# Performance work log

Measured on AMD Instinct MI355X. Metric: run time of the kernel, lower is better.

Reference implementation:

```python
import jax, jax.numpy as jnp
import numpy as np

IN_DIMS = 512
TOKEN_DIM = 512
NUM_HEADS = 1
D = TOKEN_DIM * NUM_HEADS
SCALE = TOKEN_DIM ** (-0.5)
EPS = 1e-12  # torch F.normalize default


def _l2norm(v, axis):
    n = jnp.sqrt(jnp.sum(v * v, axis=axis, keepdims=True))
    return v / jnp.maximum(n, EPS)


def setup_inputs() -> dict:
    key = jax.random.key(0)
    ks = jax.random.split(key, 10)
    B, C, H, W = 64, IN_DIMS, 28, 28
    s_in = IN_DIMS ** -0.5
    s_d = D ** -0.5
    return {
        "x": jax.random.normal(ks[0], (B, C, H, W), jnp.float32),
        "Wq": jax.random.normal(ks[1], (IN_DIMS, D), jnp.float32) * s_in,
        "bq": jax.random.normal(ks[2], (D,), jnp.float32) * 0.01,
        "Wk": jax.random.normal(ks[3], (IN_DIMS, D), jnp.float32) * s_in,
        "bk": jax.random.normal(ks[4], (D,), jnp.float32) * 0.01,
        "w_g": jax.random.normal(ks[5], (D, 1), jnp.float32),
        "Wp": jax.random.normal(ks[6], (D, D), jnp.float32) * s_d,
        "bp": jax.random.normal(ks[7], (D,), jnp.float32) * 0.01,
        "Wf": jax.random.normal(ks[8], (D, TOKEN_DIM), jnp.float32) * s_d,
        "bf": jax.random.normal(ks[9], (TOKEN_DIM,), jnp.float32) * 0.01,
    }


def reference(x, Wq, bq, Wk, bk, w_g, Wp, bp, Wf, bf):
    B, C, H, W = x.shape
    t = x.reshape(B, C, H * W).transpose(0, 2, 1)          # [B, N, C]
    query = _l2norm(t @ Wq + bq, axis=-1)                  # [B, N, D]
    k = _l2norm(t @ Wk + bk, axis=-1)                      # [B, N, D]
    attn = _l2norm((query @ w_g) * SCALE, axis=1)          # [B, N, 1], normalized over tokens
    ctx = jnp.sum(attn * query, axis=1, keepdims=True)     # [B, 1, D] global context
    out = (ctx * k) @ Wp + bp + query                      # [B, N, D]
    out = out @ Wf + bf                                    # [B, N, TOKEN_DIM]
    return out.transpose(0, 2, 1).reshape(B, -1, H, W)
```

## Files before the change

kernel.cpp:

```cpp
#include <hip/hip_runtime.h>

#define EPSN 1e-12f
#define SCALE_F 0.044194173824159216f
#define MTOT 50176

typedef __bf16 bf16x8 __attribute__((ext_vector_type(8)));
typedef __bf16 bf16x4 __attribute__((ext_vector_type(4)));
typedef float  f32x4  __attribute__((ext_vector_type(4)));

__device__ __forceinline__ void gld16(const void* src, void* dst) {
  __builtin_amdgcn_global_load_lds(
      (const __attribute__((address_space(1))) unsigned int*)src,
      (__attribute__((address_space(3))) unsigned int*)dst, 16, 0, 0);
}

__global__ __launch_bounds__(256) void k_prep_t(const float* __restrict__ Wq,
                                                const float* __restrict__ Wk,
                                                __bf16* __restrict__ WqT,
                                                __bf16* __restrict__ WkT) {
  __shared__ float Tq[32][33], Tk[32][33];
  const int c0 = blockIdx.x * 32, d0 = blockIdx.y * 32;
  const int dx = threadIdx.x, cy = threadIdx.y;
  #pragma unroll
  for (int p = 0; p < 4; ++p) {
    int c = cy + p * 8;
    Tq[c][dx] = Wq[(size_t)(c0 + c) * 512 + d0 + dx];
    Tk[c][dx] = Wk[(size_t)(c0 + c) * 512 + d0 + dx];
  }
  __syncthreads();
  #pragma unroll
  for (int p = 0; p < 4; ++p) {
    int d = cy + p * 8;
    WqT[(size_t)(d0 + d) * 512 + c0 + dx] = (__bf16)Tq[dx][d];
    WkT[(size_t)(d0 + d) * 512 + c0 + dx] = (__bf16)Tk[dx][d];
  }
}

__global__ __launch_bounds__(512) void k_prep_w(const float* __restrict__ Wp,
                                                const float* __restrict__ Wf,
                                                const float* __restrict__ bp,
                                                const float* __restrict__ bfv,
                                                __bf16* __restrict__ WcT,
                                                float* __restrict__ bpf) {
  const int kk0 = blockIdx.x * 8;
  const int d = threadIdx.x;
  float acc[8] = {};
  float bacc = 0.f;
  const bool dobp = (blockIdx.x == 0);
  for (int c = 0; c < 512; ++c) {
    float wf = Wf[(size_t)c * 512 + d];
    #pragma unroll
    for (int i = 0; i < 8; ++i) acc[i] = fmaf(Wp[(size_t)(kk0 + i) * 512 + c], wf, acc[i]);
    if (dobp) bacc = fmaf(bp[c], wf, bacc);
  }
  #pragma unroll
  for (int i = 0; i < 8; ++i) {
    WcT[(size_t)d * 1024 + kk0 + i]       = (__bf16)acc[i];
    WcT[(size_t)d * 1024 + 512 + kk0 + i] = (__bf16)Wf[(size_t)(kk0 + i) * 512 + d];
  }
  if (dobp) bpf[d] = bacc + bfv[d];
}

__global__ __launch_bounds__(256, 3) void k_gemm(const float* __restrict__ x,
                                                 const __bf16* __restrict__ WqT,
                                                 const __bf16* __restrict__ WkT,
                                                 const float* __restrict__ bq,
                                                 const float* __restrict__ bk,
                                                 const float* __restrict__ wg,
                                                 __bf16* __restrict__ qraw,
                                                 __bf16* __restrict__ kraw,
                                                 float* __restrict__ psqQ,
                                                 float* __restrict__ psqK,
                                                 float* __restrict__ gdo) {
  __shared__ __align__(1024) unsigned char As[8192], Bs[8192];
  const int t = threadIdx.x, l = t & 63, w = t >> 6;
  const int li = l & 15, lq = l >> 4;
  const int p = blockIdx.x;
  const int xq = p & 7, q2 = p >> 3;
  const int m8 = q2 & 7;
  const int g = (q2 >> 3) * 8 + xq;
  const int b = g / 7, mt = g % 7;
  const int qk = m8 >> 2, nt = m8 & 3;
  const int m0 = mt * 128;
  const __bf16* Wt = qk ? WkT : WqT;

  const int r0 = 2 * w, r1 = r0 + 1;
  int row0 = m0 + r0 * 16 + li; if (row0 > 783) row0 = 783;
  int row1 = m0 + r1 * 16 + li; if (row1 > 783) row1 = 783;
  const float* xp0 = x + ((size_t)b * 512 + lq * 8) * 784 + row0;
  const float* xp1 = x + ((size_t)b * 512 + lq * 8) * 784 + row1;
  const __bf16* wp0 = Wt + (size_t)(nt * 128 + r0 * 16 + li) * 512 + lq * 8;
  const __bf16* wp1 = Wt + (size_t)(nt * 128 + r1 * 16 + li) * 512 + lq * 8;

  f32x4 acc[4][4] = {};

  for (int ks = 0; ks < 16; ++ks) {
    const int k0 = ks * 32;
    gld16(wp0 + k0, Bs + r0 * 1024);
    gld16(wp1 + k0, Bs + r1 * 1024);
    {
      float v0[8], v1[8];
      #pragma unroll
      for (int j = 0; j < 8; ++j) v0[j] = xp0[(size_t)(k0 + j) * 784];
      #pragma unroll
      for (int j = 0; j < 8; ++j) v1[j] = xp1[(size_t)(k0 + j) * 784];
      bf16x8 a0, a1;
      #pragma unroll
      for (int j = 0; j < 8; ++j) { a0[j] = (__bf16)v0[j]; a1[j] = (__bf16)v1[j]; }
      *(bf16x8*)(As + r0 * 1024 + l * 16) = a0;
      *(bf16x8*)(As + r1 * 1024 + l * 16) = a1;
    }
    __syncthreads();
    bf16x8 af[4];
    #pragma unroll
    for (int rb = 0; rb < 4; ++rb)
      af[rb] = *(const bf16x8*)(As + ((w & 1) * 4 + rb) * 1024 + l * 16);
    #pragma unroll
    for (int cb = 0; cb < 4; ++cb) {
      bf16x8 bf = *(const bf16x8*)(Bs + ((w >> 1) * 4 + cb) * 1024 + l * 16);
      #pragma unroll
      for (int rb = 0; rb < 4; ++rb)
        acc[rb][cb] = __builtin_amdgcn_mfma_f32_16x16x32_bf16(af[rb], bf, acc[rb][cb], 0, 0, 0);
    }
    __syncthreads();
  }

  const float* bias = qk ? bk : bq;
  __bf16* dst = qk ? kraw : qraw;
  float* psq = qk ? psqK : psqQ;
  const int colb = nt * 128 + (w >> 1) * 64;
  const int cg = nt * 2 + (w >> 1);
  float bv[4], wv[4];
  #pragma unroll
  for (int cb = 0; cb < 4; ++cb) {
    int col = colb + cb * 16 + li;
    bv[cb] = bias[col];
    wv[cb] = qk ? 0.f : wg[col];
  }
  #pragma unroll
  for (int rb = 0; rb < 4; ++rb)
    #pragma unroll
    for (int j = 0; j < 4; ++j) {
      int rowg = m0 + (w & 1) * 64 + rb * 16 + lq * 4 + j;
      bool ok = rowg < 784;
      size_t token = (size_t)b * 784 + rowg;
      float ss = 0.f, sg = 0.f;
      #pragma unroll
      for (int cb = 0; cb < 4; ++cb) {
        float v = acc[rb][cb][j] + bv[cb];
        ss = fmaf(v, v, ss);
        sg = fmaf(v, wv[cb], sg);
        if (ok) dst[token * 512 + colb + cb * 16 + li] = (__bf16)v;
      }
      ss += __shfl_xor(ss, 1); ss += __shfl_xor(ss, 2); ss += __shfl_xor(ss, 4); ss += __shfl_xor(ss, 8);
      sg += __shfl_xor(sg, 1); sg += __shfl_xor(sg, 2); sg += __shfl_xor(sg, 4); sg += __shfl_xor(sg, 8);
      if (ok && li == 0) {
        psq[(size_t)cg * MTOT + token] = ss;
        if (!qk) gdo[(size_t)cg * MTOT + token] = sg;
      }
    }
}

__global__ __launch_bounds__(256) void k_normc(const float* __restrict__ psqQ,
                                               const float* __restrict__ psqK,
                                               const float* __restrict__ gdo,
                                               float* __restrict__ invqA,
                                               float* __restrict__ invkA,
                                               float* __restrict__ coefA,
                                               float* __restrict__ gA) {
  const int tkn = blockIdx.x * 256 + threadIdx.x;
  if (tkn >= MTOT) return;
  float sq = 0.f, sk = 0.f, gd = 0.f;
  #pragma unroll
  for (int cg = 0; cg < 8; ++cg) {
    sq += psqQ[(size_t)cg * MTOT + tkn];
    sk += psqK[(size_t)cg * MTOT + tkn];
    gd += gdo[(size_t)cg * MTOT + tkn];
  }
  float invq = 1.f / fmaxf(sqrtf(sq), EPSN);
  float invk = 1.f / fmaxf(sqrtf(sk), EPSN);
  float gv = gd * invq;
  invqA[tkn] = invq;
  invkA[tkn] = invk;
  coefA[tkn] = gv * invq;
  gA[tkn]    = gv;
}

__global__ __launch_bounds__(512) void k_pctx(const __bf16* __restrict__ qraw,
                                              const float* __restrict__ coefA,
                                              const float* __restrict__ gA,
                                              float* __restrict__ ctx) {
  __shared__ float wred[8];
  const int b = blockIdx.x, t = threadIdx.x;
  const size_t base = (size_t)b * 784;
  float gsq = 0.f;
  { float gv = gA[base + t]; gsq = gv * gv; }
  if (t + 512 < 784) { float gv = gA[base + t + 512]; gsq = fmaf(gv, gv, gsq); }
  gsq += __shfl_xor(gsq, 1);  gsq += __shfl_xor(gsq, 2);  gsq += __shfl_xor(gsq, 4);
  gsq += __shfl_xor(gsq, 8);  gsq += __shfl_xor(gsq, 16); gsq += __shfl_xor(gsq, 32);
  if ((t & 63) == 0) wred[t >> 6] = gsq;
  __syncthreads();
  float tot = 0.f;
  #pragma unroll
  for (int i = 0; i < 8; ++i) tot += wred[i];
  const float alpha = SCALE_F / fmaxf(sqrtf(tot) * SCALE_F, EPSN);
  float a0 = 0.f, a1 = 0.f, a2 = 0.f, a3 = 0.f;
  for (int n = 0; n < 784; n += 4) {
    a0 = fmaf(coefA[base + n],     (float)qraw[(base + n) * 512 + t],     a0);
    a1 = fmaf(coefA[base + n + 1], (float)qraw[(base + n + 1) * 512 + t], a1);
    a2 = fmaf(coefA[base + n + 2], (float)qraw[(base + n + 2) * 512 + t], a2);
    a3 = fmaf(coefA[base + n + 3], (float)qraw[(base + n + 3) * 512 + t], a3);
  }
  ctx[(size_t)b * 512 + t] = alpha * ((a0 + a1) + (a2 + a3));
}

__global__ __launch_bounds__(256, 3) void k_out(const __bf16* __restrict__ qraw,
                                                const __bf16* __restrict__ kraw,
                                                const float* __restrict__ invqA,
                                                const float* __restrict__ invkA,
                                                const float* __restrict__ ctx,
                                                const __bf16* __restrict__ WcT,
                                                const float* __restrict__ bpf,
                                                float* __restrict__ out) {
  __shared__ __align__(1024) unsigned char As[8192], Bs[8192];
  __shared__ float ctx_l[512];
  const int t = threadIdx.x, l = t & 63, w = t >> 6;
  const int li = l & 15, lq = l >> 4;
  const int p = blockIdx.x;
  const int xq = p & 7, q2 = p >> 3;
  const int nt = q2 & 3;
  const int g = (q2 >> 2) * 8 + xq;
  const int b = g / 7, mt = g % 7;
  const int m0 = mt * 128;

  ctx_l[t]       = ctx[(size_t)b * 512 + t];
  ctx_l[t + 256] = ctx[(size_t)b * 512 + t + 256];

  const int rA0 = w, rA1 = w + 4;
  int row0 = m0 + rA0 * 16 + li; if (row0 > 783) row0 = 783;
  int row1 = m0 + rA1 * 16 + li; if (row1 > 783) row1 = 783;
  const size_t tk0 = (size_t)b * 784 + row0, tk1 = (size_t)b * 784 + row1;
  const float iq0 = invqA[tk0], ik0 = invkA[tk0];
  const float iq1 = invqA[tk1], ik1 = invkA[tk1];
  const __bf16* wpB0 = WcT + (size_t)(nt * 128 + (2 * w) * 16 + li) * 1024 + lq * 8;
  const __bf16* wpB1 = WcT + (size_t)(nt * 128 + (2 * w + 1) * 16 + li) * 1024 + lq * 8;

  f32x4 acc[4][4] = {};
  __syncthreads();

  for (int ks = 0; ks < 32; ++ks) {
    const int k0 = ks * 32;
    gld16(wpB0 + k0, Bs + (2 * w) * 1024);
    gld16(wpB1 + k0, Bs + (2 * w + 1) * 1024);
    {
      const bool dk = ks < 16;
      const __bf16* ap = dk ? kraw : qraw;
      const int kk = (k0 & 511) + lq * 8;
      bf16x8 v0 = *(const bf16x8*)(ap + tk0 * 512 + kk);
      bf16x8 v1 = *(const bf16x8*)(ap + tk1 * 512 + kk);
      const float s0 = dk ? ik0 : iq0, s1 = dk ? ik1 : iq1;
      bf16x8 o0, o1;
      if (dk) {
        f32x4 c0 = *(const f32x4*)&ctx_l[kk];
        f32x4 c1 = *(const f32x4*)&ctx_l[kk + 4];
        #pragma unroll
        for (int j = 0; j < 4; ++j) {
          o0[j]     = (__bf16)((float)v0[j]     * s0 * c0[j]);
          o0[4 + j] = (__bf16)((float)v0[4 + j] * s0 * c1[j]);
          o1[j]     = (__bf16)((float)v1[j]     * s1 * c0[j]);
          o1[4 + j] = (__bf16)((float)v1[4 + j] * s1 * c1[j]);
        }
      } else {
        #pragma unroll
        for (int j = 0; j < 8; ++j) {
          o0[j] = (__bf16)((float)v0[j] * s0);
          o1[j] = (__bf16)((float)v1[j] * s1);
        }
      }
      *(bf16x8*)(As + rA0 * 1024 + l * 16) = o0;
      *(bf16x8*)(As + rA1 * 1024 + l * 16) = o1;
    }
    __syncthreads();
    bf16x8 af[4];
    #pragma unroll
    for (int rb = 0; rb < 4; ++rb)
      af[rb] = *(const bf16x8*)(As + ((w & 1) * 4 + rb) * 1024 + l * 16);
    #pragma unroll
    for (int cb = 0; cb < 4; ++cb) {
      bf16x8 bf = *(const bf16x8*)(Bs + ((w >> 1) * 4 + cb) * 1024 + l * 16);
      #pragma unroll
      for (int rb = 0; rb < 4; ++rb)
        acc[rb][cb] = __builtin_amdgcn_mfma_f32_16x16x32_bf16(af[rb], bf, acc[rb][cb], 0, 0, 0);
    }
    __syncthreads();
  }

  const int colb = nt * 128 + (w >> 1) * 64;
  float bv[4];
  #pragma unroll
  for (int cb = 0; cb < 4; ++cb) bv[cb] = bpf[colb + cb * 16 + li];
  #pragma unroll
  for (int rb = 0; rb < 4; ++rb) {
    int nrow = m0 + (w & 1) * 64 + rb * 16 + lq * 4;
    if (nrow < 784) {
      #pragma unroll
      for (int cb = 0; cb < 4; ++cb) {
        f32x4 v;
        #pragma unroll
        for (int j = 0; j < 4; ++j) v[j] = acc[rb][cb][j] + bv[cb];
        *(f32x4*)&out[((size_t)b * 512 + colb + cb * 16 + li) * 784 + nrow] = v;
      }
    }
  }
}

extern "C" void kernel_launch(void* const* d_in, const int* in_sizes, int n_in,
                              void* d_out, int out_size, void* d_ws, size_t ws_size,
                              hipStream_t stream) {
  const float* x   = (const float*)d_in[0];
  const float* Wq  = (const float*)d_in[1];
  const float* bq  = (const float*)d_in[2];
  const float* Wk  = (const float*)d_in[3];
  const float* bk  = (const float*)d_in[4];
  const float* wg  = (const float*)d_in[5];
  const float* Wp  = (const float*)d_in[6];
  const float* bp  = (const float*)d_in[7];
  const float* Wf  = (const float*)d_in[8];
  const float* bfv = (const float*)d_in[9];
  float* out = (float*)d_out;
  char* ws = (char*)d_ws;

  const size_t SZRAW = (size_t)MTOT * 512 * 2;
  size_t off = 0;
  __bf16* qraw = (__bf16*)(ws + off); off += SZRAW;
  __bf16* kraw = (__bf16*)(ws + off); off += SZRAW;
  __bf16* WqT  = (__bf16*)(ws + off); off += 524288;
  __bf16* WkT  = (__bf16*)(ws + off); off += 524288;
  __bf16* WcT  = (__bf16*)(ws + off); off += 1048576;
  float*  bpf  = (float*) (ws + off); off += 2048;
  float*  psqQ = (float*) (ws + off); off += (size_t)8 * MTOT * 4;
  float*  psqK = (float*) (ws + off); off += (size_t)8 * MTOT * 4;
  float*  gdo  = (float*) (ws + off); off += (size_t)8 * MTOT * 4;
  float*  invqA = (float*)(ws + off); off += (size_t)MTOT * 4;
  float*  invkA = (float*)(ws + off); off += (size_t)MTOT * 4;
  float*  coefA = (float*)(ws + off); off += (size_t)MTOT * 4;
  float*  gA    = (float*)(ws + off); off += (size_t)MTOT * 4;
  float*  ctx   = (float*)(ws + off); off += 131072;

  k_prep_t<<<dim3(16, 16), dim3(32, 8), 0, stream>>>(Wq, Wk, WqT, WkT);
  k_prep_w<<<dim3(64),     dim3(512),   0, stream>>>(Wp, Wf, bp, bfv, WcT, bpf);
  k_gemm  <<<dim3(3584),   dim3(256),   0, stream>>>(x, WqT, WkT, bq, bk, wg,
                                                     qraw, kraw, psqQ, psqK, gdo);
  k_normc <<<dim3(196),    dim3(256),   0, stream>>>(psqQ, psqK, gdo, invqA, invkA, coefA, gA);
  k_pctx  <<<dim3(64),     dim3(512),   0, stream>>>(qraw, coefA, gA, ctx);
  k_out   <<<dim3(1792),   dim3(256),   0, stream>>>(qraw, kraw, invqA, invkA, ctx, WcT, bpf, out);
}
```

Baseline: 411.3 us.

## Pre-transpose x to bf16, fuse Q/K GEMMs, and split ctx reduction

Adds a transpose kernel that writes x as token-major bf16 in two half-batch chunks. The GEMM then loads A tiles with direct global-to-LDS loads instead of strided fp32 loads plus conversion. The GEMM now computes Q and K together from one shared A tile, halving the number of x reads at the cost of doubled accumulators, higher register pressure and occupancy lowered to 2. The context kernel is split across 4 channel chunks and 4 token slices per batch to expose more parallelism. The risk is the extra round trip through the transpose buffer.

```diff
diff --git a/kernel.cpp b/kernel.cpp
--- a/kernel.cpp
+++ b/kernel.cpp
@@ -5,13 +5,33 @@
 #define MTOT 50176
 
 typedef __bf16 bf16x8 __attribute__((ext_vector_type(8)));
-typedef __bf16 bf16x4 __attribute__((ext_vector_type(4)));
 typedef float  f32x4  __attribute__((ext_vector_type(4)));
 
 __device__ __forceinline__ void gld16(const void* src, void* dst) {
   __builtin_amdgcn_global_load_lds(
       (const __attribute__((address_space(1))) unsigned int*)src,
       (__attribute__((address_space(3))) unsigned int*)dst, 16, 0, 0);
+}
+
+__global__ __launch_bounds__(256) void k_xt(const float* __restrict__ x,
+                                            __bf16* __restrict__ xT, int b0) {
+  __shared__ float T[32][33];
+  const int n0 = blockIdx.x * 32, c0 = blockIdx.y * 32;
+  const int bl = blockIdx.z, b = b0 + bl;
+  const int dx = threadIdx.x, ty = threadIdx.y;
+  #pragma unroll
+  for (int pp = 0; pp < 4; ++pp) {
+    int c = ty + pp * 8;
+    int n = n0 + dx;
+    T[c][dx] = (n < 784) ? x[((size_t)b * 512 + c0 + c) * 784 + n] : 0.f;
+  }
+  __syncthreads();
+  #pragma unroll
+  for (int pp = 0; pp < 4; ++pp) {
+    int n = ty + pp * 8;
+    if (n0 + n < 784)
+      xT[((size_t)bl * 784 + n0 + n) * 512 + c0 + dx] = (__bf16)T[dx][n];
+  }
 }
 
 __global__ __launch_bounds__(256) void k_prep_t(const float* __restrict__ Wq,
@@ -61,55 +81,49 @@
   if (dobp) bpf[d] = bacc + bfv[d];
 }
 
-__global__ __launch_bounds__(256, 3) void k_gemm(const float* __restrict__ x,
+__global__ __launch_bounds__(256, 2) void k_gemm(const __bf16* __restrict__ xT,
                                                  const __bf16* __restrict__ WqT,
                                                  const __bf16* __restrict__ WkT,
                                                  const float* __restrict__ bq,
                                                  const float* __restrict__ bk,
                                                  const float* __restrict__ wg,
+                                                 const int b0,
                                                  __bf16* __restrict__ qraw,
                                                  __bf16* __restrict__ kraw,
                                                  float* __restrict__ psqQ,
                                                  float* __restrict__ psqK,
                                                  float* __restrict__ gdo) {
-  __shared__ __align__(1024) unsigned char As[8192], Bs[8192];
+  __shared__ __align__(1024) unsigned char As[8192], BQs[8192], BKs[8192];
   const int t = threadIdx.x, l = t & 63, w = t >> 6;
   const int li = l & 15, lq = l >> 4;
   const int p = blockIdx.x;
   const int xq = p & 7, q2 = p >> 3;
-  const int m8 = q2 & 7;
-  const int g = (q2 >> 3) * 8 + xq;
-  const int b = g / 7, mt = g % 7;
-  const int qk = m8 >> 2, nt = m8 & 3;
+  const int nt = q2 & 3;
+  const int g = (q2 >> 2) * 8 + xq;
+  const int bl = g / 7, mt = g % 7;
+  const int b = b0 + bl;
   const int m0 = mt * 128;
-  const __bf16* Wt = qk ? WkT : WqT;
 
   const int r0 = 2 * w, r1 = r0 + 1;
   int row0 = m0 + r0 * 16 + li; if (row0 > 783) row0 = 783;
   int row1 = m0 + r1 * 16 + li; if (row1 > 783) row1 = 783;
-  const float* xp0 = x + ((size_t)b * 512 + lq * 8) * 784 + row0;
-  const float* xp1 = x + ((size_t)b * 512 + lq * 8) * 784 + row1;
-  const __bf16* wp0 = Wt + (size_t)(nt * 128 + r0 * 16 + li) * 512 + lq * 8;
-  const __bf16* wp1 = Wt + (size_t)(nt * 128 + r1 * 16 + li) * 512 + lq * 8;
-
-  f32x4 acc[4][4] = {};
+  const __bf16* a0s = xT + ((size_t)bl * 784 + row0) * 512 + lq * 8;
+  const __bf16* a1s = xT + ((size_t)bl * 784 + row1) * 512 + lq * 8;
+  const __bf16* q0s = WqT + (size_t)(nt * 128 + r0 * 16 + li) * 512 + lq * 8;
+  const __bf16* q1s = WqT + (size_t)(nt * 128 + r1 * 16 + li) * 512 + lq * 8;
+  const __bf16* k0s = WkT + (size_t)(nt * 128 + r0 * 16 + li) * 512 + lq * 8;
+  const __bf16* k1s = WkT + (size_t)(nt * 128 + r1 * 16 + li) * 512 + lq * 8;
+
+  f32x4 accQ[4][4] = {}, accK[4][4] = {};
 
   for (int ks = 0; ks < 16; ++ks) {
     const int k0 = ks * 32;
-    gld16(wp0 + k0, Bs + r0 * 1024);
-    gld16(wp1 + k0, Bs + r1 * 1024);
-    {
-      float v0[8], v1[8];
-      #pragma unroll
-      for (int j = 0; j < 8; ++j) v0[j] = xp0[(size_t)(k0 + j) * 784];
-      #pragma unroll
-      for (int j = 0; j < 8; ++j) v1[j] = xp1[(size_t)(k0 + j) * 784];
-      bf16x8 a0, a1;
-      #pragma unroll
-      for (int j = 0; j < 8; ++j) { a0[j] = (__bf16)v0[j]; a1[j] = (__bf16)v1[j]; }
-      *(bf16x8*)(As + r0 * 1024 + l * 16) = a0;
-      *(bf16x8*)(As + r1 * 1024 + l * 16) = a1;
-    }
+    gld16(a0s + k0, As + r0 * 1024);
+    gld16(a1s + k0, As + r1 * 1024);
+    gld16(q0s + k0, BQs + r0 * 1024);
+    gld16(q1s + k0, BQs + r1 * 1024);
+    gld16(k0s + k0, BKs + r0 * 1024);
+    gld16(k1s + k0, BKs + r1 * 1024);
     __syncthreads();
     bf16x8 af[4];
     #pragma unroll
@@ -117,25 +131,25 @@
       af[rb] = *(const bf16x8*)(As + ((w & 1) * 4 + rb) * 1024 + l * 16);
     #pragma unroll
     for (int cb = 0; cb < 4; ++cb) {
-      bf16x8 bf = *(const bf16x8*)(Bs + ((w >> 1) * 4 + cb) * 1024 + l * 16);
+      bf16x8 bq8 = *(const bf16x8*)(BQs + ((w >> 1) * 4 + cb) * 1024 + l * 16);
       #pragma unroll
       for (int rb = 0; rb < 4; ++rb)
-        acc[rb][cb] = __builtin_amdgcn_mfma_f32_16x16x32_bf16(af[rb], bf, acc[rb][cb], 0, 0, 0);
+        accQ[rb][cb] = __builtin_amdgcn_mfma_f32_16x16x32_bf16(af[rb], bq8, accQ[rb][cb], 0, 0, 0);
+      bf16x8 bk8 = *(const bf16x8*)(BKs + ((w >> 1) * 4 + cb) * 1024 + l * 16);
+      #pragma unroll
+      for (int rb = 0; rb < 4; ++rb)
+        accK[rb][cb] = __builtin_amdgcn_mfma_f32_16x16x32_bf16(af[rb], bk8, accK[rb][cb], 0, 0, 0);
     }
     __syncthreads();
   }
 
-  const float* bias = qk ? bk : bq;
-  __bf16* dst = qk ? kraw : qraw;
-  float* psq = qk ? psqK : psqQ;
   const int colb = nt * 128 + (w >> 1) * 64;
   const int cg = nt * 2 + (w >> 1);
-  float bv[4], wv[4];
+  float bqv[4], bkv[4], wv[4];
   #pragma unroll
   for (int cb = 0; cb < 4; ++cb) {
     int col = colb + cb * 16 + li;
-    bv[cb] = bias[col];
-    wv[cb] = qk ? 0.f : wg[col];
+    bqv[cb] = bq[col]; bkv[cb] = bk[col]; wv[cb] = wg[col];
   }
   #pragma unroll
   for (int rb = 0; rb < 4; ++rb)
@@ -144,19 +158,26 @@
       int rowg = m0 + (w & 1) * 64 + rb * 16 + lq * 4 + j;
       bool ok = rowg < 784;
       size_t token = (size_t)b * 784 + rowg;
-      float ss = 0.f, sg = 0.f;
+      float ssq = 0.f, ssk = 0.f, sg = 0.f;
       #pragma unroll
       for (int cb = 0; cb < 4; ++cb) {
-        float v = acc[rb][cb][j] + bv[cb];
-        ss = fmaf(v, v, ss);
-        sg = fmaf(v, wv[cb], sg);
-        if (ok) dst[token * 512 + colb + cb * 16 + li] = (__bf16)v;
+        float vq = accQ[rb][cb][j] + bqv[cb];
+        float vk = accK[rb][cb][j] + bkv[cb];
+        ssq = fmaf(vq, vq, ssq);
+        ssk = fmaf(vk, vk, ssk);
+        sg  = fmaf(vq, wv[cb], sg);
+        if (ok) {
+          qraw[token * 512 + colb + cb * 16 + li] = (__bf16)vq;
+          kraw[token * 512 + colb + cb * 16 + li] = (__bf16)vk;
+        }
       }
-      ss += __shfl_xor(ss, 1); ss += __shfl_xor(ss, 2); ss += __shfl_xor(ss, 4); ss += __shfl_xor(ss, 8);
-      sg += __shfl_xor(sg, 1); sg += __shfl_xor(sg, 2); sg += __shfl_xor(sg, 4); sg += __shfl_xor(sg, 8);
+      ssq += __shfl_xor(ssq, 1); ssq += __shfl_xor(ssq, 2); ssq += __shfl_xor(ssq, 4); ssq += __shfl_xor(ssq, 8);
+      ssk += __shfl_xor(ssk, 1); ssk += __shfl_xor(ssk, 2); ssk += __shfl_xor(ssk, 4); ssk += __shfl_xor(ssk, 8);
+      sg  += __shfl_xor(sg, 1);  sg  += __shfl_xor(sg, 2);  sg  += __shfl_xor(sg, 4);  sg  += __shfl_xor(sg, 8);
       if (ok && li == 0) {
-        psq[(size_t)cg * MTOT + token] = ss;
-        if (!qk) gdo[(size_t)cg * MTOT + token] = sg;
+        psqQ[(size_t)cg * MTOT + token] = ssq;
+        psqK[(size_t)cg * MTOT + token] = ssk;
+        gdo [(size_t)cg * MTOT + token] = sg;
       }
     }
 }
@@ -191,9 +212,10 @@
                                               const float* __restrict__ gA,
                                               float* __restrict__ ctx) {
   __shared__ float wred[8];
-  const int b = blockIdx.x, t = threadIdx.x;
+  __shared__ float part[4][128];
+  const int ch = blockIdx.x, b = blockIdx.y, t = threadIdx.x;
   const size_t base = (size_t)b * 784;
-  float gsq = 0.f;
+  float gsq;
   { float gv = gA[base + t]; gsq = gv * gv; }
   if (t + 512 < 784) { float gv = gA[base + t + 512]; gsq = fmaf(gv, gv, gsq); }
   gsq += __shfl_xor(gsq, 1);  gsq += __shfl_xor(gsq, 2);  gsq += __shfl_xor(gsq, 4);
@@ -204,14 +226,23 @@
   #pragma unroll
   for (int i = 0; i < 8; ++i) tot += wred[i];
   const float alpha = SCALE_F / fmaxf(sqrtf(tot) * SCALE_F, EPSN);
+  const int dof = t & 127, s = t >> 7;
+  const int nb = s * 196;
+  const __bf16* qb = qraw + (base + nb) * 512 + ch * 128 + dof;
+  const float* cf = coefA + base + nb;
   float a0 = 0.f, a1 = 0.f, a2 = 0.f, a3 = 0.f;
-  for (int n = 0; n < 784; n += 4) {
-    a0 = fmaf(coefA[base + n],     (float)qraw[(base + n) * 512 + t],     a0);
-    a1 = fmaf(coefA[base + n + 1], (float)qraw[(base + n + 1) * 512 + t], a1);
-    a2 = fmaf(coefA[base + n + 2], (float)qraw[(base + n + 2) * 512 + t], a2);
-    a3 = fmaf(coefA[base + n + 3], (float)qraw[(base + n + 3) * 512 + t], a3);
-  }
-  ctx[(size_t)b * 512 + t] = alpha * ((a0 + a1) + (a2 + a3));
+  for (int n = 0; n < 196; n += 4) {
+    a0 = fmaf(cf[n],     (float)qb[(size_t)n * 512],       a0);
+    a1 = fmaf(cf[n + 1], (float)qb[(size_t)(n + 1) * 512], a1);
+    a2 = fmaf(cf[n + 2], (float)qb[(size_t)(n + 2) * 512], a2);
+    a3 = fmaf(cf[n + 3], (float)qb[(size_t)(n + 3) * 512], a3);
+  }
+  part[s][dof] = (a0 + a1) + (a2 + a3);
+  __syncthreads();
+  if (t < 128) {
+    float sum = part[0][t] + part[1][t] + part[2][t] + part[3][t];
+    ctx[(size_t)b * 512 + ch * 128 + t] = alpha * sum;
+  }
 }
 
 __global__ __launch_bounds__(256, 3) void k_out(const __bf16* __restrict__ qraw,
@@ -331,9 +362,11 @@
   char* ws = (char*)d_ws;
 
   const size_t SZRAW = (size_t)MTOT * 512 * 2;
+  const size_t SZXT  = (size_t)32 * 784 * 512 * 2;
   size_t off = 0;
   __bf16* qraw = (__bf16*)(ws + off); off += SZRAW;
   __bf16* kraw = (__bf16*)(ws + off); off += SZRAW;
+  __bf16* xT   = (__bf16*)(ws + off); off += SZXT;
   __bf16* WqT  = (__bf16*)(ws + off); off += 524288;
   __bf16* WkT  = (__bf16*)(ws + off); off += 524288;
   __bf16* WcT  = (__bf16*)(ws + off); off += 1048576;
@@ -349,9 +382,12 @@
 
   k_prep_t<<<dim3(16, 16), dim3(32, 8), 0, stream>>>(Wq, Wk, WqT, WkT);
   k_prep_w<<<dim3(64),     dim3(512),   0, stream>>>(Wp, Wf, bp, bfv, WcT, bpf);
-  k_gemm  <<<dim3(3584),   dim3(256),   0, stream>>>(x, WqT, WkT, bq, bk, wg,
-                                                     qraw, kraw, psqQ, psqK, gdo);
-  k_normc <<<dim3(196),    dim3(256),   0, stream>>>(psqQ, psqK, gdo, invqA, invkA, coefA, gA);
-  k_pctx  <<<dim3(64),     dim3(512),   0, stream>>>(qraw, coefA, gA, ctx);
-  k_out   <<<dim3(1792),   dim3(256),   0, stream>>>(qraw, kraw, invqA, invkA, ctx, WcT, bpf, out);
-}
+  for (int s = 0; s < 2; ++s) {
+    k_xt  <<<dim3(25, 16, 32), dim3(32, 8), 0, stream>>>(x, xT, s * 32);
+    k_gemm<<<dim3(896),        dim3(256),   0, stream>>>(xT, WqT, WkT, bq, bk, wg, s * 32,
+                                                         qraw, kraw, psqQ, psqK, gdo);
+  }
+  k_normc<<<dim3(196),   dim3(256), 0, stream>>>(psqQ, psqK, gdo, invqA, invkA, coefA, gA);
+  k_pctx <<<dim3(4, 64), dim3(512), 0, stream>>>(qraw, coefA, gA, ctx);
+  k_out  <<<dim3(1792),  dim3(256), 0, stream>>>(qraw, kraw, invqA, invkA, ctx, WcT, bpf, out);
+}
```

Result: no change. 408.8 us (-0.6%).
